# Optimization experiments

Measured on AMD Instinct MI355X. Metric: run time of the kernel, lower is better.

The kernel has to match this reference:

```python
import jax, jax.numpy as jnp
import numpy as np

N, M, H, K, CIN, COUT, P = 50000, 50000, 32, 15, 64, 128, 3
KP_EXTENT = 0.072
RADIUS = 0.06


def setup_inputs() -> dict:
    key = jax.random.key(0)
    ks = jax.random.split(key, 7)
    q_pts = jax.random.uniform(ks[0], (N, P), dtype=jnp.float32) * 0.05
    s_pts = jax.random.uniform(ks[1], (M, P), dtype=jnp.float32) * 0.05
    neighb_inds = jax.random.randint(ks[2], (N, H), 0, M, dtype=jnp.int64)
    x = jax.random.normal(ks[3], (M, CIN), dtype=jnp.float32)
    # kernel points inside sphere of radius RADIUS (stand-in for load_kernels)
    kernel_points = jax.random.normal(ks[4], (K, P), dtype=jnp.float32) * (0.5 * RADIUS)
    stddev = np.sqrt(1.0 / (K * COUT)).astype(np.float32)
    weights = jax.random.normal(ks[5], (K, CIN, COUT), dtype=jnp.float32) * stddev
    bias = jnp.zeros((COUT,), dtype=jnp.float32)
    return {"q_pts": q_pts, "s_pts": s_pts, "neighb_inds": neighb_inds,
            "x": x, "kernel_points": kernel_points, "weights": weights, "bias": bias}


def reference(q_pts, s_pts, neighb_inds, x, kernel_points, weights, bias):
    # pad support points with a far-away point and features with a zero row
    s_pad = jnp.concatenate([s_pts, jnp.full((1, s_pts.shape[1]), 1e6, s_pts.dtype)], axis=0)
    x_pad = jnp.concatenate([x, jnp.zeros((1, x.shape[1]), x.dtype)], axis=0)
    # gather neighbor coords/features: [N, H, P], [N, H, CIN]
    neighbors = s_pad[neighb_inds] - q_pts[:, None, :]
    neighb_x = x_pad[neighb_inds]
    # distances to kernel points: [N, H, K]
    diff = neighbors[:, :, None, :] - kernel_points  # [N, H, K, P]
    sq_d = jnp.sum(diff * diff, axis=-1)
    all_weights = jax.nn.relu(1.0 - jnp.sqrt(sq_d) / KP_EXTENT)  # linear influence
    # aggregate: [N, K, CIN] then apply per-kernel-point weights and sum over K
    weighted_features = jnp.einsum('nhk,nhc->nkc', all_weights, neighb_x)
    out = jnp.einsum('nkc,kco->no', weighted_features, weights) + bias  # [N, COUT]
    return out
```

## Files before the change

### kernel.cpp

```cpp
#include <hip/hip_runtime.h>
#include <hip/hip_bf16.h>


#define NPTS   50000
#define NPAD   50048
#define HNB    32
#define KPTS   15
#define CING   64
#define COUTG  128
#define KDIM   960
#define MSUP   50000
#define INV_EXT 13.888889f

typedef __attribute__((ext_vector_type(8))) short bf16x8;
typedef __attribute__((ext_vector_type(8))) unsigned short u16x8;
typedef __attribute__((ext_vector_type(4))) float f32x4;

static __device__ __forceinline__ unsigned short f2bf(float f) {
    unsigned int u = __float_as_uint(f);
    u += 0x7FFFu + ((u >> 16) & 1u);
    return (unsigned short)(u >> 16);
}

__global__ __launch_bounds__(256) void kpconv_x2bf(const float* __restrict__ x,
                                                   unsigned short* __restrict__ xb) {
    int i = (blockIdx.x * 256 + threadIdx.x) * 8;
    if (i >= MSUP * CING) return;
    float4 a = *(const float4*)(x + i);
    float4 b = *(const float4*)(x + i + 4);
    u16x8 o;
    o[0] = f2bf(a.x); o[1] = f2bf(a.y); o[2] = f2bf(a.z); o[3] = f2bf(a.w);
    o[4] = f2bf(b.x); o[5] = f2bf(b.y); o[6] = f2bf(b.z); o[7] = f2bf(b.w);
    *(u16x8*)(xb + i) = o;
}

__global__ void kpconv_wt(const float* __restrict__ wgt, unsigned short* __restrict__ Wt) {
    int kc = blockIdx.x;
    int o  = threadIdx.x;
    Wt[(size_t)o * KDIM + kc] = f2bf(wgt[(size_t)kc * COUTG + o]);
}

__global__ __launch_bounds__(256) void kpconv_agg2(
    const float* __restrict__ q_pts, const float* __restrict__ s_pts,
    const int* __restrict__ inds, const unsigned short* __restrict__ xb,
    const float* __restrict__ kpts, unsigned short* __restrict__ wf)
{
    __shared__ float4 nb4[4][HNB];

    const int tid  = threadIdx.x;
    const int g    = tid >> 6;
    const int lane = tid & 63;
    const int l15  = lane & 15;
    const int quad = lane >> 4;
    const int n    = blockIdx.x * 4 + g;

    if (lane < HNB) {
        int m = inds[n * HNB + lane];
        float qx = q_pts[n * 3 + 0];
        float qy = q_pts[n * 3 + 1];
        float qz = q_pts[n * 3 + 2];
        nb4[g][lane] = make_float4(s_pts[m * 3 + 0] - qx,
                                   s_pts[m * 3 + 1] - qy,
                                   s_pts[m * 3 + 2] - qz,
                                   __int_as_float(m));
    }
    __syncthreads();

    const bool kvalid = (l15 < KPTS);
    const int  kidx   = kvalid ? l15 : 0;
    const float kx = kpts[kidx * 3 + 0];
    const float ky = kpts[kidx * 3 + 1];
    const float kz = kpts[kidx * 3 + 2];

    bf16x8 af;
    int mrow[8];
#pragma unroll
    for (int j = 0; j < 8; ++j) {
        float4 v = nb4[g][quad * 8 + j];
        mrow[j] = __float_as_int(v.w);
        float dx = v.x - kx, dy = v.y - ky, dz = v.z - kz;
        float d  = sqrtf(dx * dx + dy * dy + dz * dz);
        float w  = kvalid ? fmaxf(0.f, 1.f - d * INV_EXT) : 0.f;
        af[j] = (short)f2bf(w);
    }

    f32x4 acc[4];
#pragma unroll
    for (int nt = 0; nt < 4; ++nt) acc[nt] = (f32x4){0.f, 0.f, 0.f, 0.f};

#pragma unroll
    for (int nt = 0; nt < 4; ++nt) {
        const int c = nt * 16 + l15;
        bf16x8 bfr;
#pragma unroll
        for (int j = 0; j < 8; ++j)
            bfr[j] = (short)xb[((size_t)mrow[j] << 6) + c];
        acc[nt] = __builtin_amdgcn_mfma_f32_16x16x32_bf16(af, bfr, acc[nt], 0, 0, 0);
    }

    const size_t base = (size_t)n * KDIM;
#pragma unroll
    for (int nt = 0; nt < 4; ++nt) {
        const int c = nt * 16 + l15;
#pragma unroll
        for (int r = 0; r < 4; ++r) {
            int k = quad * 4 + r;
            if (k < KPTS) wf[base + k * CING + c] = f2bf(acc[nt][r]);
        }
    }
}

#define GBM 64
#define GBK 64
#define GLP 72

__global__ __launch_bounds__(256) void kpconv_gemm2(
    const unsigned short* __restrict__ A,
    const unsigned short* __restrict__ Bt,
    const float* __restrict__ bias,
    float* __restrict__ out)
{
    __shared__ unsigned short As[GBM * GLP];
    __shared__ unsigned short Bs[COUTG * GLP];

    const int tid  = threadIdx.x;
    const int wave = tid >> 6;
    const int lane = tid & 63;
    const int l15  = lane & 15;
    const int quad = lane >> 4;
    const long blockM = (long)blockIdx.x * GBM;

    f32x4 acc[8];
#pragma unroll
    for (int i = 0; i < 8; ++i) acc[i] = (f32x4){0.f, 0.f, 0.f, 0.f};

    const int arow = tid >> 2, acol = (tid & 3) * 16;
    const int brow = tid >> 1, bcol = (tid & 1) * 32;
    const unsigned short* aptr = A + (size_t)(blockM + arow) * KDIM + acol;
    const unsigned short* bptr = Bt + (size_t)brow * KDIM + bcol;

    uint4 ra0 = *(const uint4*)(aptr);
    uint4 ra1 = *(const uint4*)(aptr + 8);
    uint4 rb0 = *(const uint4*)(bptr);
    uint4 rb1 = *(const uint4*)(bptr + 8);
    uint4 rb2 = *(const uint4*)(bptr + 16);
    uint4 rb3 = *(const uint4*)(bptr + 24);

    for (int kk = 0; kk < KDIM; kk += GBK) {
        __syncthreads();
        *(uint4*)&As[arow * GLP + acol]      = ra0;
        *(uint4*)&As[arow * GLP + acol + 8]  = ra1;
        *(uint4*)&Bs[brow * GLP + bcol]      = rb0;
        *(uint4*)&Bs[brow * GLP + bcol + 8]  = rb1;
        *(uint4*)&Bs[brow * GLP + bcol + 16] = rb2;
        *(uint4*)&Bs[brow * GLP + bcol + 24] = rb3;
        __syncthreads();

        if (kk + GBK < KDIM) {
            ra0 = *(const uint4*)(aptr + kk + GBK);
            ra1 = *(const uint4*)(aptr + kk + GBK + 8);
            rb0 = *(const uint4*)(bptr + kk + GBK);
            rb1 = *(const uint4*)(bptr + kk + GBK + 8);
            rb2 = *(const uint4*)(bptr + kk + GBK + 16);
            rb3 = *(const uint4*)(bptr + kk + GBK + 24);
        }

#pragma unroll
        for (int ch = 0; ch < 2; ++ch) {
            bf16x8 afr = *(bf16x8*)&As[(wave * 16 + l15) * GLP + ch * 32 + quad * 8];
#pragma unroll
            for (int nf = 0; nf < 8; ++nf) {
                bf16x8 bfr = *(bf16x8*)&Bs[(nf * 16 + l15) * GLP + ch * 32 + quad * 8];
                acc[nf] = __builtin_amdgcn_mfma_f32_16x16x32_bf16(afr, bfr, acc[nf], 0, 0, 0);
            }
        }
    }

    const long r0 = blockM + wave * 16 + quad * 4;
#pragma unroll
    for (int nf = 0; nf < 8; ++nf) {
        const int col = nf * 16 + l15;
        const float bv = bias[col];
#pragma unroll
        for (int r = 0; r < 4; ++r) {
            long row = r0 + r;
            if (row < NPTS) out[row * COUTG + col] = acc[nf][r] + bv;
        }
    }
}

extern "C" void kernel_launch(void* const* d_in, const int* in_sizes, int n_in,
                              void* d_out, int out_size, void* d_ws, size_t ws_size,
                              hipStream_t stream) {
    const float* q_pts = (const float*)d_in[0];
    const float* s_pts = (const float*)d_in[1];
    const int*   inds  = (const int*)d_in[2];
    const float* x     = (const float*)d_in[3];
    const float* kpts  = (const float*)d_in[4];
    const float* wgt   = (const float*)d_in[5];
    const float* bias  = (const float*)d_in[6];
    float* out = (float*)d_out;

    unsigned short* wf = (unsigned short*)d_ws;
    unsigned short* xb = wf + (size_t)NPAD * KDIM;
    unsigned short* Wt = xb + (size_t)MSUP * CING;

    kpconv_x2bf<<<(MSUP * CING / 8 + 255) / 256, 256, 0, stream>>>(x, xb);
    kpconv_wt<<<KDIM, COUTG, 0, stream>>>(wgt, Wt);
    kpconv_agg2<<<NPTS / 4, 256, 0, stream>>>(q_pts, s_pts, inds, xb, kpts, wf);
    kpconv_gemm2<<<NPAD / GBM, 256, 0, stream>>>(wf, Wt, bias, out);
}
```

Measured before the change: 159.5 us.

## Vectorize neighbor feature gather via LDS transpose and pad K to 16 per channel

Aggregation now gathers each neighbor's 64 bf16 features with 16-byte loads into a per-wave LDS tile transposed to channel-major, then feeds MFMA from LDS instead of scalar 2-byte global gathers. The intermediate weighted-feature layout becomes channel-major with kernel points padded to 16, enabling packed 8-byte stores, and the weight transpose is zero-padded to match. The two prep kernels are merged into one launch. This adds extra GEMM work for the padded K dimension, a larger intermediate buffer, and extra block syncs.

After: 159.7 us. About the same (+0.1%).

```diff
diff --git a/kernel.cpp b/kernel.cpp
--- a/kernel.cpp
+++ b/kernel.cpp
@@ -8,12 +8,11 @@
 #define KPTS   15
 #define CING   64
 #define COUTG  128
-#define KDIM   960
+#define KDIM2  1024
 #define MSUP   50000
 #define INV_EXT 13.888889f
 
 typedef __attribute__((ext_vector_type(8))) short bf16x8;
-typedef __attribute__((ext_vector_type(8))) unsigned short u16x8;
 typedef __attribute__((ext_vector_type(4))) float f32x4;
 
 static __device__ __forceinline__ unsigned short f2bf(float f) {
@@ -22,47 +21,61 @@
     return (unsigned short)(u >> 16);
 }
 
-__global__ __launch_bounds__(256) void kpconv_x2bf(const float* __restrict__ x,
-                                                   unsigned short* __restrict__ xb) {
-    int i = (blockIdx.x * 256 + threadIdx.x) * 8;
-    if (i >= MSUP * CING) return;
-    float4 a = *(const float4*)(x + i);
-    float4 b = *(const float4*)(x + i + 4);
-    u16x8 o;
-    o[0] = f2bf(a.x); o[1] = f2bf(a.y); o[2] = f2bf(a.z); o[3] = f2bf(a.w);
-    o[4] = f2bf(b.x); o[5] = f2bf(b.y); o[6] = f2bf(b.z); o[7] = f2bf(b.w);
-    *(u16x8*)(xb + i) = o;
-}
-
-__global__ void kpconv_wt(const float* __restrict__ wgt, unsigned short* __restrict__ Wt) {
-    int kc = blockIdx.x;
-    int o  = threadIdx.x;
-    Wt[(size_t)o * KDIM + kc] = f2bf(wgt[(size_t)kc * COUTG + o]);
-}
-
-__global__ __launch_bounds__(256) void kpconv_agg2(
+#define XBLKS 1563
+__global__ __launch_bounds__(256) void kpconv_prep(
+    const float* __restrict__ x, const float* __restrict__ wgt,
+    unsigned short* __restrict__ xb, unsigned short* __restrict__ Wt2)
+{
+    int b = blockIdx.x;
+    if (b < XBLKS) {
+        int i = (b * 256 + threadIdx.x) * 8;
+        if (i < MSUP * CING) {
+            float4 a = *(const float4*)(x + i);
+            float4 c = *(const float4*)(x + i + 4);
+            unsigned short o[8];
+            o[0]=f2bf(a.x); o[1]=f2bf(a.y); o[2]=f2bf(a.z); o[3]=f2bf(a.w);
+            o[4]=f2bf(c.x); o[5]=f2bf(c.y); o[6]=f2bf(c.z); o[7]=f2bf(c.w);
+            uint4 p;
+            p.x = o[0] | (o[1]<<16); p.y = o[2] | (o[3]<<16);
+            p.z = o[4] | (o[5]<<16); p.w = o[6] | (o[7]<<16);
+            *(uint4*)(xb + i) = p;
+        }
+    } else {
+        int e = (b - XBLKS) * 256 + threadIdx.x;
+        int o = e >> 10, j = e & 1023;
+        int c = j >> 4, k = j & 15;
+        Wt2[(size_t)o * KDIM2 + j] =
+            (k < KPTS) ? f2bf(wgt[((size_t)k * CING + c) * COUTG + o]) : (unsigned short)0;
+    }
+}
+
+#define HP 36
+
+__global__ __launch_bounds__(256) void kpconv_agg3(
     const float* __restrict__ q_pts, const float* __restrict__ s_pts,
     const int* __restrict__ inds, const unsigned short* __restrict__ xb,
     const float* __restrict__ kpts, unsigned short* __restrict__ wf)
 {
-    __shared__ float4 nb4[4][HNB];
+    __shared__ float4 nbs[8][HNB];
+    __shared__ unsigned short xls[4][CING * HP];
 
     const int tid  = threadIdx.x;
-    const int g    = tid >> 6;
+    const int wave = tid >> 6;
     const int lane = tid & 63;
     const int l15  = lane & 15;
     const int quad = lane >> 4;
-    const int n    = blockIdx.x * 4 + g;
-
-    if (lane < HNB) {
-        int m = inds[n * HNB + lane];
+
+    {
+        int p = tid >> 5, h = tid & 31;
+        int n = blockIdx.x * 8 + p;
+        int m = inds[n * HNB + h];
         float qx = q_pts[n * 3 + 0];
         float qy = q_pts[n * 3 + 1];
         float qz = q_pts[n * 3 + 2];
-        nb4[g][lane] = make_float4(s_pts[m * 3 + 0] - qx,
-                                   s_pts[m * 3 + 1] - qy,
-                                   s_pts[m * 3 + 2] - qz,
-                                   __int_as_float(m));
+        nbs[p][h] = make_float4(s_pts[m * 3 + 0] - qx,
+                                s_pts[m * 3 + 1] - qy,
+                                s_pts[m * 3 + 2] - qz,
+                                __int_as_float(m));
     }
     __syncthreads();
 
@@ -72,40 +85,79 @@
     const float ky = kpts[kidx * 3 + 1];
     const float kz = kpts[kidx * 3 + 2];
 
-    bf16x8 af;
-    int mrow[8];
-#pragma unroll
-    for (int j = 0; j < 8; ++j) {
-        float4 v = nb4[g][quad * 8 + j];
-        mrow[j] = __float_as_int(v.w);
-        float dx = v.x - kx, dy = v.y - ky, dz = v.z - kz;
-        float d  = sqrtf(dx * dx + dy * dy + dz * dz);
-        float w  = kvalid ? fmaxf(0.f, 1.f - d * INV_EXT) : 0.f;
-        af[j] = (short)f2bf(w);
-    }
-
-    f32x4 acc[4];
-#pragma unroll
-    for (int nt = 0; nt < 4; ++nt) acc[nt] = (f32x4){0.f, 0.f, 0.f, 0.f};
-
-#pragma unroll
-    for (int nt = 0; nt < 4; ++nt) {
-        const int c = nt * 16 + l15;
-        bf16x8 bfr;
-#pragma unroll
-        for (int j = 0; j < 8; ++j)
-            bfr[j] = (short)xb[((size_t)mrow[j] << 6) + c];
-        acc[nt] = __builtin_amdgcn_mfma_f32_16x16x32_bf16(af, bfr, acc[nt], 0, 0, 0);
-    }
-
-    const size_t base = (size_t)n * KDIM;
-#pragma unroll
-    for (int nt = 0; nt < 4; ++nt) {
-        const int c = nt * 16 + l15;
-#pragma unroll
-        for (int r = 0; r < 4; ++r) {
-            int k = quad * 4 + r;
-            if (k < KPTS) wf[base + k * CING + c] = f2bf(acc[nt][r]);
+    const int mch  = lane & 7;
+    const int hrow = lane >> 3;
+
+    uint4 g[2][4];
+#pragma unroll
+    for (int pp = 0; pp < 2; ++pp) {
+        int p = wave * 2 + pp;
+#pragma unroll
+        for (int i = 0; i < 4; ++i) {
+            int m = __float_as_int(nbs[p][hrow + 8 * i].w);
+            g[pp][i] = *(const uint4*)(xb + ((size_t)m << 6) + mch * 8);
+        }
+    }
+
+    bf16x8 af[2];
+#pragma unroll
+    for (int pp = 0; pp < 2; ++pp) {
+        int p = wave * 2 + pp;
+#pragma unroll
+        for (int j = 0; j < 8; ++j) {
+            float4 v = nbs[p][quad * 8 + j];
+            float dx = v.x - kx, dy = v.y - ky, dz = v.z - kz;
+            float d  = sqrtf(dx * dx + dy * dy + dz * dz);
+            float w  = kvalid ? fmaxf(0.f, 1.f - d * INV_EXT) : 0.f;
+            af[pp][j] = (short)f2bf(w);
+        }
+    }
+
+    unsigned short* X = xls[wave];
+
+#pragma unroll
+    for (int pp = 0; pp < 2; ++pp) {
+        const int n = blockIdx.x * 8 + wave * 2 + pp;
+
+#pragma unroll
+        for (int i = 0; i < 4; ++i) {
+            int h  = hrow + 8 * i;
+            int cb = mch * 8;
+            unsigned int d0 = g[pp][i].x, d1 = g[pp][i].y,
+                         d2 = g[pp][i].z, d3 = g[pp][i].w;
+            X[(cb + 0) * HP + h] = (unsigned short)(d0);
+            X[(cb + 1) * HP + h] = (unsigned short)(d0 >> 16);
+            X[(cb + 2) * HP + h] = (unsigned short)(d1);
+            X[(cb + 3) * HP + h] = (unsigned short)(d1 >> 16);
+            X[(cb + 4) * HP + h] = (unsigned short)(d2);
+            X[(cb + 5) * HP + h] = (unsigned short)(d2 >> 16);
+            X[(cb + 6) * HP + h] = (unsigned short)(d3);
+            X[(cb + 7) * HP + h] = (unsigned short)(d3 >> 16);
+        }
+        __syncthreads();
+
+        f32x4 acc[4];
+#pragma unroll
+        for (int nt = 0; nt < 4; ++nt) acc[nt] = (f32x4){0.f, 0.f, 0.f, 0.f};
+
+#pragma unroll
+        for (int nt = 0; nt < 4; ++nt) {
+            int c = l15 + 16 * nt;
+            bf16x8 bfr;
+            ((uint2*)&bfr)[0] = *(const uint2*)&X[c * HP + quad * 8];
+            ((uint2*)&bfr)[1] = *(const uint2*)&X[c * HP + quad * 8 + 4];
+            acc[nt] = __builtin_amdgcn_mfma_f32_16x16x32_bf16(af[pp], bfr, acc[nt], 0, 0, 0);
+        }
+        __syncthreads();
+
+        const size_t base = (size_t)n * KDIM2;
+#pragma unroll
+        for (int nt = 0; nt < 4; ++nt) {
+            int c = l15 + 16 * nt;
+            uint2 pk;
+            pk.x = f2bf(acc[nt][0]) | ((unsigned int)f2bf(acc[nt][1]) << 16);
+            pk.y = f2bf(acc[nt][2]) | ((unsigned int)f2bf(acc[nt][3]) << 16);
+            *(uint2*)(wf + base + c * 16 + quad * 4) = pk;
         }
     }
 }
@@ -114,7 +166,7 @@
 #define GBK 64
 #define GLP 72
 
-__global__ __launch_bounds__(256) void kpconv_gemm2(
+__global__ __launch_bounds__(256) void kpconv_gemm3(
     const unsigned short* __restrict__ A,
     const unsigned short* __restrict__ Bt,
     const float* __restrict__ bias,
@@ -136,8 +188,8 @@
 
     const int arow = tid >> 2, acol = (tid & 3) * 16;
     const int brow = tid >> 1, bcol = (tid & 1) * 32;
-    const unsigned short* aptr = A + (size_t)(blockM + arow) * KDIM + acol;
-    const unsigned short* bptr = Bt + (size_t)brow * KDIM + bcol;
+    const unsigned short* aptr = A + (size_t)(blockM + arow) * KDIM2 + acol;
+    const unsigned short* bptr = Bt + (size_t)brow * KDIM2 + bcol;
 
     uint4 ra0 = *(const uint4*)(aptr);
     uint4 ra1 = *(const uint4*)(aptr + 8);
@@ -146,7 +198,7 @@
     uint4 rb2 = *(const uint4*)(bptr + 16);
     uint4 rb3 = *(const uint4*)(bptr + 24);
 
-    for (int kk = 0; kk < KDIM; kk += GBK) {
+    for (int kk = 0; kk < KDIM2; kk += GBK) {
         __syncthreads();
         *(uint4*)&As[arow * GLP + acol]      = ra0;
         *(uint4*)&As[arow * GLP + acol + 8]  = ra1;
@@ -156,7 +208,7 @@
         *(uint4*)&Bs[brow * GLP + bcol + 24] = rb3;
         __syncthreads();
 
-        if (kk + GBK < KDIM) {
+        if (kk + GBK < KDIM2) {
             ra0 = *(const uint4*)(aptr + kk + GBK);
             ra1 = *(const uint4*)(aptr + kk + GBK + 8);
             rb0 = *(const uint4*)(bptr + kk + GBK);
@@ -202,11 +254,10 @@
     float* out = (float*)d_out;
 
     unsigned short* wf = (unsigned short*)d_ws;
-    unsigned short* xb = wf + (size_t)NPAD * KDIM;
-    unsigned short* Wt = xb + (size_t)MSUP * CING;
-
-    kpconv_x2bf<<<(MSUP * CING / 8 + 255) / 256, 256, 0, stream>>>(x, xb);
-    kpconv_wt<<<KDIM, COUTG, 0, stream>>>(wgt, Wt);
-    kpconv_agg2<<<NPTS / 4, 256, 0, stream>>>(q_pts, s_pts, inds, xb, kpts, wf);
-    kpconv_gemm2<<<NPAD / GBM, 256, 0, stream>>>(wf, Wt, bias, out);
-}
+    unsigned short* xb = wf + (size_t)NPAD * KDIM2;
+    unsigned short* Wt2 = xb + (size_t)MSUP * CING;
+
+    kpconv_prep<<<XBLKS + 512, 256, 0, stream>>>(x, wgt, xb, Wt2);
+    kpconv_agg3<<<NPTS / 8, 256, 0, stream>>>(q_pts, s_pts, inds, xb, kpts, wf);
+    kpconv_gemm3<<<NPAD / GBM, 256, 0, stream>>>(wf, Wt2, bias, out);
+}
```

## Fuse aggregation and output GEMM into one kernel via LDS-resident weighted features

Applied to the files above, without the earlier changes.

Merges the per-point neighbour aggregation and the dense output GEMM into a single kernel. Each block handles 16 query points, keeps the bf16 weighted features in LDS in a k-padded (16 kernel points) channel-major layout, then multiplies them against a re-laid-out weight matrix read directly from global memory. The two prep kernels are also merged into one launch. This removes the global round trip of the ~96 MB intermediate and two launches. In exchange it adds padded-K GEMM work and global weight loads per block with no LDS staging.

New measurement: 202.3 us. +26.8%, slower.

```diff
diff --git a/kernel.cpp b/kernel.cpp
--- a/kernel.cpp
+++ b/kernel.cpp
@@ -3,17 +3,18 @@
 
 
 #define NPTS   50000
-#define NPAD   50048
 #define HNB    32
 #define KPTS   15
 #define CING   64
 #define COUTG  128
-#define KDIM   960
+#define KDIM2  1024
 #define MSUP   50000
 #define INV_EXT 13.888889f
 
+#define PTS_BLK 16
+#define PITCH   1040
+
 typedef __attribute__((ext_vector_type(8))) short bf16x8;
-typedef __attribute__((ext_vector_type(8))) unsigned short u16x8;
 typedef __attribute__((ext_vector_type(4))) float f32x4;
 
 static __device__ __forceinline__ unsigned short f2bf(float f) {
@@ -22,47 +23,63 @@
     return (unsigned short)(u >> 16);
 }
 
-__global__ __launch_bounds__(256) void kpconv_x2bf(const float* __restrict__ x,
-                                                   unsigned short* __restrict__ xb) {
-    int i = (blockIdx.x * 256 + threadIdx.x) * 8;
-    if (i >= MSUP * CING) return;
-    float4 a = *(const float4*)(x + i);
-    float4 b = *(const float4*)(x + i + 4);
-    u16x8 o;
-    o[0] = f2bf(a.x); o[1] = f2bf(a.y); o[2] = f2bf(a.z); o[3] = f2bf(a.w);
-    o[4] = f2bf(b.x); o[5] = f2bf(b.y); o[6] = f2bf(b.z); o[7] = f2bf(b.w);
-    *(u16x8*)(xb + i) = o;
+#define XBLKS 1563
+__global__ __launch_bounds__(256) void kpconv_prep(
+    const float* __restrict__ x, const float* __restrict__ wgt,
+    unsigned short* __restrict__ xb, unsigned short* __restrict__ Wt2)
+{
+    int b = blockIdx.x;
+    if (b < XBLKS) {
+        int i = (b * 256 + threadIdx.x) * 8;
+        if (i < MSUP * CING) {
+            float4 a = *(const float4*)(x + i);
+            float4 c = *(const float4*)(x + i + 4);
+            unsigned short o[8];
+            o[0]=f2bf(a.x); o[1]=f2bf(a.y); o[2]=f2bf(a.z); o[3]=f2bf(a.w);
+            o[4]=f2bf(c.x); o[5]=f2bf(c.y); o[6]=f2bf(c.z); o[7]=f2bf(c.w);
+            uint4 p;
+            p.x = o[0] | (o[1]<<16); p.y = o[2] | (o[3]<<16);
+            p.z = o[4] | (o[5]<<16); p.w = o[6] | (o[7]<<16);
+            *(uint4*)(xb + i) = p;
+        }
+    } else {
+        int e = (b - XBLKS) * 256 + threadIdx.x;
+        int o = e >> 10, j = e & 1023;
+        int c = j >> 4, k = j & 15;
+        Wt2[(size_t)o * KDIM2 + j] =
+            (k < KPTS) ? f2bf(wgt[((size_t)k * CING + c) * COUTG + o]) : (unsigned short)0;
+    }
 }
 
-__global__ void kpconv_wt(const float* __restrict__ wgt, unsigned short* __restrict__ Wt) {
-    int kc = blockIdx.x;
-    int o  = threadIdx.x;
-    Wt[(size_t)o * KDIM + kc] = f2bf(wgt[(size_t)kc * COUTG + o]);
-}
-
-__global__ __launch_bounds__(256) void kpconv_agg2(
+__global__ __launch_bounds__(256) void kpconv_fused(
     const float* __restrict__ q_pts, const float* __restrict__ s_pts,
     const int* __restrict__ inds, const unsigned short* __restrict__ xb,
-    const float* __restrict__ kpts, unsigned short* __restrict__ wf)
+    const float* __restrict__ kpts, const unsigned short* __restrict__ Wt2,
+    const float* __restrict__ bias, float* __restrict__ out)
 {
-    __shared__ float4 nb4[4][HNB];
+    __shared__ float nbx[PTS_BLK][HNB];
+    __shared__ float nby[PTS_BLK][HNB];
+    __shared__ float nbz[PTS_BLK][HNB];
+    __shared__ int   sidx[PTS_BLK][HNB];
+    __shared__ unsigned short wfT[PTS_BLK * PITCH];
 
     const int tid  = threadIdx.x;
-    const int g    = tid >> 6;
+    const int wave = tid >> 6;
     const int lane = tid & 63;
     const int l15  = lane & 15;
     const int quad = lane >> 4;
-    const int n    = blockIdx.x * 4 + g;
+    const int n0   = blockIdx.x * PTS_BLK;
 
-    if (lane < HNB) {
-        int m = inds[n * HNB + lane];
-        float qx = q_pts[n * 3 + 0];
-        float qy = q_pts[n * 3 + 1];
-        float qz = q_pts[n * 3 + 2];
-        nb4[g][lane] = make_float4(s_pts[m * 3 + 0] - qx,
-                                   s_pts[m * 3 + 1] - qy,
-                                   s_pts[m * 3 + 2] - qz,
-                                   __int_as_float(m));
+#pragma unroll
+    for (int pq = 0; pq < 2; ++pq) {
+        const int p = wave * 4 + pq * 2 + (lane >> 5);
+        const int h = lane & 31;
+        const int n = n0 + p;
+        const int m = inds[n * HNB + h];
+        sidx[p][h] = m;
+        nbx[p][h] = s_pts[(size_t)m * 3 + 0] - q_pts[n * 3 + 0];
+        nby[p][h] = s_pts[(size_t)m * 3 + 1] - q_pts[n * 3 + 1];
+        nbz[p][h] = s_pts[(size_t)m * 3 + 2] - q_pts[n * 3 + 2];
     }
     __syncthreads();
 
@@ -72,119 +89,75 @@
     const float ky = kpts[kidx * 3 + 1];
     const float kz = kpts[kidx * 3 + 2];
 
-    bf16x8 af;
-    int mrow[8];
 #pragma unroll
-    for (int j = 0; j < 8; ++j) {
-        float4 v = nb4[g][quad * 8 + j];
-        mrow[j] = __float_as_int(v.w);
-        float dx = v.x - kx, dy = v.y - ky, dz = v.z - kz;
-        float d  = sqrtf(dx * dx + dy * dy + dz * dz);
-        float w  = kvalid ? fmaxf(0.f, 1.f - d * INV_EXT) : 0.f;
-        af[j] = (short)f2bf(w);
-    }
+    for (int pp = 0; pp < 4; ++pp) {
+        const int p = wave * 4 + pp;
 
-    f32x4 acc[4];
+        int mrow[8];
 #pragma unroll
-    for (int nt = 0; nt < 4; ++nt) acc[nt] = (f32x4){0.f, 0.f, 0.f, 0.f};
+        for (int j = 0; j < 8; ++j) mrow[j] = sidx[p][quad * 8 + j];
 
+        unsigned short bv[4][8];
 #pragma unroll
-    for (int nt = 0; nt < 4; ++nt) {
-        const int c = nt * 16 + l15;
-        bf16x8 bfr;
+        for (int nt = 0; nt < 4; ++nt) {
+            const int c = nt * 16 + l15;
 #pragma unroll
-        for (int j = 0; j < 8; ++j)
-            bfr[j] = (short)xb[((size_t)mrow[j] << 6) + c];
-        acc[nt] = __builtin_amdgcn_mfma_f32_16x16x32_bf16(af, bfr, acc[nt], 0, 0, 0);
-    }
+            for (int j = 0; j < 8; ++j)
+                bv[nt][j] = xb[((size_t)mrow[j] << 6) + c];
+        }
 
-    const size_t base = (size_t)n * KDIM;
+        bf16x8 af;
 #pragma unroll
-    for (int nt = 0; nt < 4; ++nt) {
-        const int c = nt * 16 + l15;
-#pragma unroll
-        for (int r = 0; r < 4; ++r) {
-            int k = quad * 4 + r;
-            if (k < KPTS) wf[base + k * CING + c] = f2bf(acc[nt][r]);
-        }
-    }
-}
-
-#define GBM 64
-#define GBK 64
-#define GLP 72
-
-__global__ __launch_bounds__(256) void kpconv_gemm2(
-    const unsigned short* __restrict__ A,
-    const unsigned short* __restrict__ Bt,
-    const float* __restrict__ bias,
-    float* __restrict__ out)
-{
-    __shared__ unsigned short As[GBM * GLP];
-    __shared__ unsigned short Bs[COUTG * GLP];
-
-    const int tid  = threadIdx.x;
-    const int wave = tid >> 6;
-    const int lane = tid & 63;
-    const int l15  = lane & 15;
-    const int quad = lane >> 4;
-    const long blockM = (long)blockIdx.x * GBM;
-
-    f32x4 acc[8];
-#pragma unroll
-    for (int i = 0; i < 8; ++i) acc[i] = (f32x4){0.f, 0.f, 0.f, 0.f};
-
-    const int arow = tid >> 2, acol = (tid & 3) * 16;
-    const int brow = tid >> 1, bcol = (tid & 1) * 32;
-    const unsigned short* aptr = A + (size_t)(blockM + arow) * KDIM + acol;
-    const unsigned short* bptr = Bt + (size_t)brow * KDIM + bcol;
-
-    uint4 ra0 = *(const uint4*)(aptr);
-    uint4 ra1 = *(const uint4*)(aptr + 8);
-    uint4 rb0 = *(const uint4*)(bptr);
-    uint4 rb1 = *(const uint4*)(bptr + 8);
-    uint4 rb2 = *(const uint4*)(bptr + 16);
-    uint4 rb3 = *(const uint4*)(bptr + 24);
-
-    for (int kk = 0; kk < KDIM; kk += GBK) {
-        __syncthreads();
-        *(uint4*)&As[arow * GLP + acol]      = ra0;
-        *(uint4*)&As[arow * GLP + acol + 8]  = ra1;
-        *(uint4*)&Bs[brow * GLP + bcol]      = rb0;
-        *(uint4*)&Bs[brow * GLP + bcol + 8]  = rb1;
-        *(uint4*)&Bs[brow * GLP + bcol + 16] = rb2;
-        *(uint4*)&Bs[brow * GLP + bcol + 24] = rb3;
-        __syncthreads();
-
-        if (kk + GBK < KDIM) {
-            ra0 = *(const uint4*)(aptr + kk + GBK);
-            ra1 = *(const uint4*)(aptr + kk + GBK + 8);
-            rb0 = *(const uint4*)(bptr + kk + GBK);
-            rb1 = *(const uint4*)(bptr + kk + GBK + 8);
-            rb2 = *(const uint4*)(bptr + kk + GBK + 16);
-            rb3 = *(const uint4*)(bptr + kk + GBK + 24);
+        for (int j = 0; j < 8; ++j) {
+            const int h = quad * 8 + j;
+            float dx = nbx[p][h] - kx;
+            float dy = nby[p][h] - ky;
+            float dz = nbz[p][h] - kz;
+            float d  = sqrtf(dx * dx + dy * dy + dz * dz);
+            float w  = kvalid ? fmaxf(0.f, 1.f - d * INV_EXT) : 0.f;
+            af[j] = (short)f2bf(w);
         }
 
 #pragma unroll
-        for (int ch = 0; ch < 2; ++ch) {
-            bf16x8 afr = *(bf16x8*)&As[(wave * 16 + l15) * GLP + ch * 32 + quad * 8];
+        for (int nt = 0; nt < 4; ++nt) {
+            bf16x8 bfr;
 #pragma unroll
-            for (int nf = 0; nf < 8; ++nf) {
-                bf16x8 bfr = *(bf16x8*)&Bs[(nf * 16 + l15) * GLP + ch * 32 + quad * 8];
-                acc[nf] = __builtin_amdgcn_mfma_f32_16x16x32_bf16(afr, bfr, acc[nf], 0, 0, 0);
-            }
+            for (int j = 0; j < 8; ++j) bfr[j] = (short)bv[nt][j];
+            f32x4 acc = (f32x4){0.f, 0.f, 0.f, 0.f};
+            acc = __builtin_amdgcn_mfma_f32_16x16x32_bf16(af, bfr, acc, 0, 0, 0);
+            uint2 pk;
+            pk.x = f2bf(acc[0]) | ((unsigned int)f2bf(acc[1]) << 16);
+            pk.y = f2bf(acc[2]) | ((unsigned int)f2bf(acc[3]) << 16);
+            *(uint2*)&wfT[p * PITCH + (nt * 16 + l15) * 16 + quad * 4] = pk;
         }
     }
+    __syncthreads();
 
-    const long r0 = blockM + wave * 16 + quad * 4;
+    f32x4 acc2[2];
+    acc2[0] = (f32x4){0.f, 0.f, 0.f, 0.f};
+    acc2[1] = (f32x4){0.f, 0.f, 0.f, 0.f};
+
+    const int col0 = wave * 32 + l15;
+    const unsigned short* bp0 = Wt2 + (size_t)col0 * KDIM2 + quad * 8;
+    const unsigned short* bp1 = bp0 + 16 * KDIM2;
+
+#pragma unroll 4
+    for (int ks = 0; ks < 32; ++ks) {
+        bf16x8 afr = *(bf16x8*)&wfT[l15 * PITCH + ks * 32 + quad * 8];
+        bf16x8 b0  = *(const bf16x8*)(bp0 + ks * 32);
+        bf16x8 b1  = *(const bf16x8*)(bp1 + ks * 32);
+        acc2[0] = __builtin_amdgcn_mfma_f32_16x16x32_bf16(afr, b0, acc2[0], 0, 0, 0);
+        acc2[1] = __builtin_amdgcn_mfma_f32_16x16x32_bf16(afr, b1, acc2[1], 0, 0, 0);
+    }
+
 #pragma unroll
-    for (int nf = 0; nf < 8; ++nf) {
-        const int col = nf * 16 + l15;
-        const float bv = bias[col];
+    for (int nf = 0; nf < 2; ++nf) {
+        const int col = col0 + nf * 16;
+        const float bvs = bias[col];
 #pragma unroll
         for (int r = 0; r < 4; ++r) {
-            long row = r0 + r;
-            if (row < NPTS) out[row * COUTG + col] = acc[nf][r] + bv;
+            const int row = n0 + quad * 4 + r;
+            out[(size_t)row * COUTG + col] = acc2[nf][r] + bvs;
         }
     }
 }
@@ -201,12 +174,10 @@
     const float* bias  = (const float*)d_in[6];
     float* out = (float*)d_out;
 
-    unsigned short* wf = (unsigned short*)d_ws;
-    unsigned short* xb = wf + (size_t)NPAD * KDIM;
-    unsigned short* Wt = xb + (size_t)MSUP * CING;
+    unsigned short* xb  = (unsigned short*)d_ws;
+    unsigned short* Wt2 = xb + (size_t)MSUP * CING;
 
-    kpconv_x2bf<<<(MSUP * CING / 8 + 255) / 256, 256, 0, stream>>>(x, xb);
-    kpconv_wt<<<KDIM, COUTG, 0, stream>>>(wgt, Wt);
-    kpconv_agg2<<<NPTS / 4, 256, 0, stream>>>(q_pts, s_pts, inds, xb, kpts, wf);
-    kpconv_gemm2<<<NPAD / GBM, 256, 0, stream>>>(wf, Wt, bias, out);
+    kpconv_prep<<<XBLKS + 512, 256, 0, stream>>>(x, wgt, xb, Wt2);
+    kpconv_fused<<<NPTS / PTS_BLK, 256, 0, stream>>>(q_pts, s_pts, inds, xb,
+                                                     kpts, Wt2, bias, out);
 }
```
